# Optimization experiments

Hardware: AMD Instinct MI355X
Metric: run time of the kernel (lower is better)

## Reference

```python
import jax, jax.numpy as jnp
import numpy as np

B, D, C, T = 2, 1024, 256, 32
H = 8
F = C // H
E = 1024  # time_embed_dim
GROUPS = 32
SCALE = F ** -0.5


def group_norm(x, scale, bias):
    # x: [B, D, C, T]; GroupNorm(32, C) over (channels-in-group, T)
    b, d, c, t = x.shape
    xg = x.reshape(b, d, GROUPS, c // GROUPS, t)
    m = xg.mean(axis=(3, 4), keepdims=True)
    v = xg.var(axis=(3, 4), keepdims=True)
    xn = ((xg - m) * jax.lax.rsqrt(v + 1e-5)).reshape(b, d, c, t)
    return xn * scale[None, None, :, None] + bias[None, None, :, None]


def rpe_R(temb, pairwise, dw, db, tw, tb, ow, ob):
    # pairwise: [B, T, T] int -> R: [B, T, T, H, F]
    pd = pairwise.astype(jnp.float32)
    dist_embs = jnp.stack([
        jnp.log1p(jnp.maximum(pd, 0.0)),
        jnp.log1p(jnp.maximum(-pd, 0.0)),
        (pairwise == 0).astype(jnp.float32),
    ], axis=-1)  # [B, T, T, 3]
    emb = (temb @ tw.T + tb)[:, :, None, :] + (dist_embs @ dw.T + db)  # [B,T,T,C]
    r = jax.nn.silu(emb) @ ow.T + ob
    return r.reshape(r.shape[0], r.shape[1], r.shape[2], H, F)


def setup_inputs() -> dict:
    key = jax.random.key(0)
    ks = jax.random.split(key, 20)
    s = 0.02
    inp = {
        "x": jax.random.normal(ks[0], (B, D, C, T), jnp.float32),
        "temb": jax.random.normal(ks[1], (B, T, E), jnp.float32),
        "norm_scale": jnp.ones((C,), jnp.float32),
        "norm_bias": jnp.zeros((C,), jnp.float32),
        "qkv_w": jax.random.normal(ks[2], (3 * C, C), jnp.float32) * s,
        "qkv_b": jnp.zeros((3 * C,), jnp.float32),
        "proj_w": jax.random.normal(ks[3], (C, C), jnp.float32) * s,
        "proj_b": jnp.zeros((C,), jnp.float32),
        # stacked RPE params for (q, k, v) nets
        "rpe_dist_w": jax.random.normal(ks[4], (3, C, 3), jnp.float32) * s,
        "rpe_dist_b": jnp.zeros((3, C), jnp.float32),
        "rpe_time_w": jax.random.normal(ks[5], (3, C, E), jnp.float32) * s,
        "rpe_time_b": jnp.zeros((3, C), jnp.float32),
        "rpe_out_w": jax.random.normal(ks[6], (3, C, C), jnp.float32) * s,
        "rpe_out_b": jax.random.normal(ks[7], (3, C), jnp.float32) * s,
        "frame_indices": jnp.sort(jax.random.randint(ks[8], (B, T), 0, 100), axis=-1),
    }
    return inp


def reference(x, temb, norm_scale, norm_bias, qkv_w, qkv_b, proj_w, proj_b,
              rpe_dist_w, rpe_dist_b, rpe_time_w, rpe_time_b, rpe_out_w, rpe_out_b,
              frame_indices):
    xn = group_norm(x, norm_scale, norm_bias)          # [B,D,C,T]
    xt = jnp.einsum('BDCT->BDTC', xn)                  # [B,D,T,C]
    qkv = (xt @ qkv_w.T + qkv_b).reshape(B, D, T, 3, H, F)
    qkv = jnp.einsum('BDTtHF->tBDHTF', qkv)
    q, k, v = qkv[0] * SCALE, qkv[1], qkv[2]           # [B,D,H,T,F]

    attn = jnp.einsum('bdhtf,bdhsf->bdhts', q, k)

    pairwise = frame_indices[:, :, None] - frame_indices[:, None, :]  # [B,T,T]
    R_q = rpe_R(temb, pairwise, rpe_dist_w[0], rpe_dist_b[0], rpe_time_w[0], rpe_time_b[0], rpe_out_w[0], rpe_out_b[0])
    R_k = rpe_R(temb, pairwise, rpe_dist_w[1], rpe_dist_b[1], rpe_time_w[1], rpe_time_b[1], rpe_out_w[1], rpe_out_b[1])
    R_v = rpe_R(temb, pairwise, rpe_dist_w[2], rpe_dist_b[2], rpe_time_w[2], rpe_time_b[2], rpe_out_w[2], rpe_out_b[2])

    attn = attn + jnp.einsum('bdhtf,btshf->bdhts', q, R_k)
    # rpe_q: forward_qk on (k*scale) then transpose last two dims
    attn = attn + jnp.einsum('bdhtf,btshf->bdhts', k * SCALE, R_q).swapaxes(-1, -2)

    attn = jax.nn.softmax(attn.astype(jnp.float32), axis=-1).astype(attn.dtype)

    out = jnp.einsum('bdhts,bdhsf->bdhtf', attn, v)
    out = out + jnp.einsum('bdhts,btshf->bdhtf', attn, R_v)

    out = jnp.einsum('BDHTF->BDTHF', out).reshape(B, D, T, C)
    out = out @ proj_w.T + proj_b
    y = xt + out                                       # residual on post-norm x (as in source)
    return jnp.einsum('BDTC->BDCT', y)
```

## Files before the change

### kernel.cpp

```cpp
#include <hip/hip_runtime.h>

#define BB 2
#define DD 1024
#define CC 256
#define TT 32
#define HH 8
#define FF 32
#define EE 1024
#define SCALE 0.17677669529663687f

typedef unsigned short u16;
typedef unsigned int u32;
typedef __attribute__((ext_vector_type(8))) short s8v;
typedef __attribute__((ext_vector_type(4))) float f32x4;

static __device__ __forceinline__ float u2f(u16 u) {
  return __uint_as_float(((u32)u) << 16);
}
static __device__ __forceinline__ u16 f2u(float f) {
  u32 x = __float_as_uint(f);
  x += 0x7fffu + ((x >> 16) & 1u);
  return (u16)(x >> 16);
}
static __device__ __forceinline__ float dot2bf(u32 a, u32 b, float c) {
  float d;
  asm("v_dot2_f32_bf16 %0, %1, %2, %3" : "=v"(d) : "v"(a), "v"(b), "v"(c));
  return d;
}
#define D2(acc, a, b) acc = dot2bf(a, b, acc)

static __device__ __forceinline__ float logits_r(
    const u16* kr,
    uint4 r0, uint4 r1, uint4 r2, uint4 r3,
    uint4 r4, uint4 r5, uint4 r6, uint4 r7,
    uint4 q0, uint4 q1, uint4 q2, uint4 q3) {
  uint4 k0 = *(const uint4*)(kr + 0);
  uint4 k1 = *(const uint4*)(kr + 8);
  uint4 k2 = *(const uint4*)(kr + 16);
  uint4 k3 = *(const uint4*)(kr + 24);
  float xq = 0.f, xr = 0.f, xk = 0.f;
  D2(xq, q0.x, k0.x); D2(xq, q0.y, k0.y); D2(xq, q0.z, k0.z); D2(xq, q0.w, k0.w);
  D2(xq, q1.x, k1.x); D2(xq, q1.y, k1.y); D2(xq, q1.z, k1.z); D2(xq, q1.w, k1.w);
  D2(xq, q2.x, k2.x); D2(xq, q2.y, k2.y); D2(xq, q2.z, k2.z); D2(xq, q2.w, k2.w);
  D2(xq, q3.x, k3.x); D2(xq, q3.y, k3.y); D2(xq, q3.z, k3.z); D2(xq, q3.w, k3.w);
  D2(xr, q0.x, r0.x); D2(xr, q0.y, r0.y); D2(xr, q0.z, r0.z); D2(xr, q0.w, r0.w);
  D2(xr, q1.x, r1.x); D2(xr, q1.y, r1.y); D2(xr, q1.z, r1.z); D2(xr, q1.w, r1.w);
  D2(xr, q2.x, r2.x); D2(xr, q2.y, r2.y); D2(xr, q2.z, r2.z); D2(xr, q2.w, r2.w);
  D2(xr, q3.x, r3.x); D2(xr, q3.y, r3.y); D2(xr, q3.z, r3.z); D2(xr, q3.w, r3.w);
  D2(xk, k0.x, r4.x); D2(xk, k0.y, r4.y); D2(xk, k0.z, r4.z); D2(xk, k0.w, r4.w);
  D2(xk, k1.x, r5.x); D2(xk, k1.y, r5.y); D2(xk, k1.z, r5.z); D2(xk, k1.w, r5.w);
  D2(xk, k2.x, r6.x); D2(xk, k2.y, r6.y); D2(xk, k2.z, r6.z); D2(xk, k2.w, r6.w);
  D2(xk, k3.x, r7.x); D2(xk, k3.y, r7.y); D2(xk, k3.z, r7.z); D2(xk, k3.w, r7.w);
  return xq + xr + xk;
}

static __device__ __forceinline__ float pv_r(
    uint4 p0, uint4 p1, uint4 p2, uint4 p3,
    const u16* vr, uint4 r0, uint4 r1, uint4 r2, uint4 r3) {
  uint4 v0 = *(const uint4*)(vr + 0),  v1 = *(const uint4*)(vr + 8);
  uint4 v2 = *(const uint4*)(vr + 16), v3 = *(const uint4*)(vr + 24);
  float o = 0.f;
  D2(o, p0.x, v0.x); D2(o, p0.y, v0.y); D2(o, p0.z, v0.z); D2(o, p0.w, v0.w);
  D2(o, p1.x, v1.x); D2(o, p1.y, v1.y); D2(o, p1.z, v1.z); D2(o, p1.w, v1.w);
  D2(o, p2.x, v2.x); D2(o, p2.y, v2.y); D2(o, p2.z, v2.z); D2(o, p2.w, v2.w);
  D2(o, p3.x, v3.x); D2(o, p3.y, v3.y); D2(o, p3.z, v3.z); D2(o, p3.w, v3.w);
  D2(o, p0.x, r0.x); D2(o, p0.y, r0.y); D2(o, p0.z, r0.z); D2(o, p0.w, r0.w);
  D2(o, p1.x, r1.x); D2(o, p1.y, r1.y); D2(o, p1.z, r1.z); D2(o, p1.w, r1.w);
  D2(o, p2.x, r2.x); D2(o, p2.y, r2.y); D2(o, p2.z, r2.z); D2(o, p2.w, r2.w);
  D2(o, p3.x, r3.x); D2(o, p3.y, r3.y); D2(o, p3.z, r3.z); D2(o, p3.w, r3.w);
  return o;
}

#define LOADROW8(P, v0, v1, v2, v3, v4, v5, v6, v7)                      \
  v0 = *(const uint4*)((P) + 0);  v1 = *(const uint4*)((P) + 8);         \
  v2 = *(const uint4*)((P) + 16); v3 = *(const uint4*)((P) + 24);        \
  v4 = *(const uint4*)((P) + 32); v5 = *(const uint4*)((P) + 40);        \
  v6 = *(const uint4*)((P) + 48); v7 = *(const uint4*)((P) + 56);
#define LOADROW4(P, v0, v1, v2, v3)                                      \
  v0 = *(const uint4*)((P) + 0);  v1 = *(const uint4*)((P) + 8);         \
  v2 = *(const uint4*)((P) + 16); v3 = *(const uint4*)((P) + 24);

__global__ __launch_bounds__(256, 4) void k_f0(
    const float* __restrict__ x, const float* __restrict__ nsc,
    const float* __restrict__ nbi, u16* __restrict__ pun,
    const float* __restrict__ qw, const float* __restrict__ pw,
    const float* __restrict__ ow, const float* __restrict__ tw,
    const float* __restrict__ temb, const float* __restrict__ tb,
    const float* __restrict__ dw, const float* __restrict__ db,
    const int* __restrict__ fidx,
    u16* __restrict__ wpk2, u16* __restrict__ ppk, u16* __restrict__ opk,
    u16* __restrict__ E) {
  const int bid = blockIdx.x;
  const int tid = threadIdx.x;
  __shared__ u16 xt[TT][264];
  __shared__ float st[EE];
  __shared__ float base_s[CC];
  __shared__ int sfi[TT];

  if (bid < 2048) {
    int xcd = bid & 7, jj = bid >> 3;
    int b = xcd >> 2;
    int d = (xcd & 3) * 256 + jj;
    const size_t xbase = ((size_t)(b * DD + d)) * 8192;
    u16* xnp = pun + xbase * 2 + 8192;
    {
      const int c0 = tid >> 3, tq = tid & 7;
      for (int c = c0; c < CC; c += 32) {
        float4 v = *(const float4*)(x + xbase + (size_t)c * TT + tq * 4);
        xt[tq * 4 + 0][c] = f2u(v.x);
        xt[tq * 4 + 1][c] = f2u(v.y);
        xt[tq * 4 + 2][c] = f2u(v.z);
        xt[tq * 4 + 3][c] = f2u(v.w);
      }
    }
    __syncthreads();
    {
      const int c = tid;
      float s = 0.f, s2 = 0.f;
      for (int t = 0; t < TT; ++t) { float v = u2f(xt[t][c]); s += v; s2 += v * v; }
      s += __shfl_xor(s, 1); s2 += __shfl_xor(s2, 1);
      s += __shfl_xor(s, 2); s2 += __shfl_xor(s2, 2);
      s += __shfl_xor(s, 4); s2 += __shfl_xor(s2, 4);
      const float mean = s * (1.f / 256.f);
      const float var = s2 * (1.f / 256.f) - mean * mean;
      const float rs = rsqrtf(var + 1e-5f);
      const float scv = nsc[c] * rs;
      const float biv = nbi[c] - mean * scv;
      for (int t = 0; t < TT; ++t) xt[t][c] = f2u(u2f(xt[t][c]) * scv + biv);
    }
    __syncthreads();
#pragma unroll
    for (int it = 0; it < 4; ++it) {
      int u = it * 256 + tid;
      int t = u >> 5, c = (u & 31) * 8;
      *(uint4*)(xnp + (size_t)u * 8) = *(const uint4*)&xt[t][c];
    }
  } else if (bid < 2272) {
    int id = (bid - 2048) * 256 + tid;
    if (id < 24576) {
      int lane = id & 63, ks = (id >> 6) & 7, tile = id >> 9;
      int hh = tile / 6, r = tile % 6, sec = r >> 1, nt = r & 1;
      int nrow = sec * 256 + hh * 32 + nt * 16 + (lane & 15);
      int k = ks * 32 + (lane >> 4) * 8;
      const float* src = qw + (size_t)nrow * 256 + k;
      u16* dst = wpk2 + (size_t)id * 8;
#pragma unroll
      for (int e = 0; e < 8; ++e) dst[e] = f2u(src[e]);
    } else if (id < 32768) {
      int j = id - 24576;
      int lane = j & 63, ks = (j >> 6) & 7, nt = j >> 9;
      int row = nt * 16 + (lane & 15);
      int k = ks * 32 + (lane >> 4) * 8;
      const float* src = pw + (size_t)row * 256 + k;
      u16* dst = ppk + (size_t)j * 8;
#pragma unroll
      for (int e = 0; e < 8; ++e) dst[e] = f2u(src[e]);
    } else {
      int j = id - 32768;
      int lane = j & 63, ks = (j >> 6) & 7, g = j >> 9;
      int n = g >> 4, ntg = g & 15;
      int row = ntg * 16 + (lane & 15);
      int k = ks * 32 + (lane >> 4) * 8;
      const float* src = ow + ((size_t)n * 256 + row) * 256 + k;
      u16* dst = opk + (size_t)j * 8;
#pragma unroll
      for (int e = 0; e < 8; ++e) dst[e] = f2u(src[e]);
    }
  } else {
    int bid3 = bid - 2272;
    int t = bid3 & 31, b = (bid3 >> 5) & 1, n = bid3 >> 6;
    for (int e = tid; e < EE; e += 256)
      st[e] = temb[((size_t)b * TT + t) * EE + e];
    if (tid < TT) sfi[tid] = fidx[b * TT + tid];
    __syncthreads();
    const int g = tid & 7, cl = tid >> 3;
#pragma unroll
    for (int pass = 0; pass < 8; ++pass) {
      const int c = pass * 32 + cl;
      const float* wr = tw + ((size_t)n * 256 + c) * 1024 + g * 4;
      float acc = 0.f;
      for (int step = 0; step < 32; ++step) {
        float4 wv = *(const float4*)(wr + step * 32);
        float4 sv = *(const float4*)(st + g * 4 + step * 32);
        acc += sv.x * wv.x + sv.y * wv.y + sv.z * wv.z + sv.w * wv.w;
      }
      acc += __shfl_xor(acc, 1);
      acc += __shfl_xor(acc, 2);
      acc += __shfl_xor(acc, 4);
      if (g == 0) base_s[c] = acc;
    }
    __syncthreads();
    const int c = tid;
    float base = base_s[c] + tb[n * 256 + c] + db[n * 256 + c];
    float dw0 = dw[(n * 256 + c) * 3 + 0];
    float dw1 = dw[(n * 256 + c) * 3 + 1];
    float dw2 = dw[(n * 256 + c) * 3 + 2];
    int ft = sfi[t];
    u16* erow = E + ((size_t)n * 2048 + b * 1024 + t * 32) * 256 + c;
    for (int s = 0; s < TT; ++s) {
      int pd = ft - sfi[s];
      float d0 = log1pf((float)(pd > 0 ? pd : 0));
      float d1 = log1pf((float)(pd < 0 ? -pd : 0));
      float d2 = (pd == 0) ? 1.f : 0.f;
      float e = base + d0 * dw0 + d1 * dw1 + d2 * dw2;
      float se = e / (1.f + expf(-e));
      erow[(size_t)s * 256] = f2u(se);
    }
  }
}

__global__ __launch_bounds__(256) void k_rgemm(
    const u16* __restrict__ E, const u16* __restrict__ opk,
    const float* __restrict__ ob,
    u16* __restrict__ RKQ, u16* __restrict__ Rv) {
  int bid = blockIdx.x;
  int n = bid >> 6, rem = bid & 63;
  int mblk = rem >> 1, nblk = rem & 1;
  int tid = threadIdx.x;
  int w = tid >> 6, lane = tid & 63;
  int l15 = lane & 15, l4 = lane >> 4;
  size_t rowbase = (size_t)n * 2048 + mblk * 64;

  f32x4 acc[2][4];
#pragma unroll
  for (int i = 0; i < 2; ++i) {
    int ntg = nblk * 8 + w * 2 + i;
    float ov = ob[n * 256 + ntg * 16 + l15];
#pragma unroll
    for (int mt = 0; mt < 4; ++mt) acc[i][mt] = (f32x4){ov, ov, ov, ov};
  }
  for (int ks = 0; ks < 8; ++ks) {
    s8v a[4];
#pragma unroll
    for (int mt = 0; mt < 4; ++mt)
      a[mt] = *(const s8v*)(E + (rowbase + mt * 16 + l15) * 256 + ks * 32 + l4 * 8);
#pragma unroll
    for (int i = 0; i < 2; ++i) {
      int ntg = nblk * 8 + w * 2 + i;
      s8v bf = *(const s8v*)(opk + (((size_t)(n * 16 + ntg) * 8 + ks) * 64 + lane) * 8);
#pragma unroll
      for (int mt = 0; mt < 4; ++mt)
        acc[i][mt] = __builtin_amdgcn_mfma_f32_16x16x32_bf16(a[mt], bf, acc[i][mt], 0, 0, 0);
    }
  }
#pragma unroll
  for (int i = 0; i < 2; ++i) {
    int cc = (nblk * 8 + w * 2 + i) * 16 + l15;
    int hh = cc >> 5, f = cc & 31;
#pragma unroll
    for (int mt = 0; mt < 4; ++mt)
#pragma unroll
      for (int r = 0; r < 4; ++r) {
        int rloc = mblk * 64 + mt * 16 + l4 * 4 + r;
        int bb2 = rloc >> 10, tt = (rloc >> 5) & 31, ss = rloc & 31;
        size_t bh = (size_t)(bb2 * 8 + hh);
        float v = acc[i][mt][r];
        if (n == 0)      RKQ[(bh * 1024 + ss * 32 + tt) * 64 + 32 + f] = f2u(v * SCALE);
        else if (n == 1) RKQ[(bh * 1024 + tt * 32 + ss) * 64 + f] = f2u(v);
        else             Rv[((bh * 32 + tt) * 32 + f) * 32 + ss] = f2u(v);
      }
  }
}

__global__ __launch_bounds__(256, 3) void k_attn(
    u16* __restrict__ pun, const u16* __restrict__ wpk2,
    const float* __restrict__ qkb,
    const u16* __restrict__ RKQ, const u16* __restrict__ Rv) {
  int bid = blockIdx.x;
  int xcd = bid & 7, i5 = bid >> 3;
  int b = xcd >> 2;
  int h = i5 & 7;
  int dg = (xcd & 3) * 64 + (i5 >> 3);
  int d0 = dg * 4;
  const int tid = threadIdx.x;
  __shared__ u16 xsbuf[32 * 264];
  __shared__ u16 qs[4][32][40];
  __shared__ u16 ks_[4][32][40];
  __shared__ u16 vT[4][32][40];
#define XS_(r, c)   xsbuf[(r) * 264 + (c)]
#define ATSP(d, t)  (xsbuf + ((d) * 32 + (t)) * 40)

  const int w = tid >> 6, lane = tid & 63;
  const int l15 = lane & 15, l4 = lane >> 4;
  const int t = tid >> 3, j = tid & 7;
  const size_t bh = (size_t)(b * 8 + h);
  const u16* rp0 = RKQ + (bh * 1024 + (size_t)t * 32 + j) * 64;
  const u16* rv0 = Rv + ((bh * 32 + (size_t)t) * 32 + j) * 32;

  u16* slot0 = pun + ((size_t)(b * DD + d0)) * 16384;

  const u16* xp0 = slot0 + 8192;
  uint4 xr0 = *(const uint4*)(xp0 + (size_t)tid * 8);
  uint4 xr1 = *(const uint4*)(xp0 + (size_t)(256 + tid) * 8);
  uint4 xr2 = *(const uint4*)(xp0 + (size_t)(512 + tid) * 8);
  uint4 xr3 = *(const uint4*)(xp0 + (size_t)(768 + tid) * 8);

  s8v wf[3][8];
#pragma unroll
  for (int i = 0; i < 3; ++i) {
    const int u = w * 3 + i;
    const int sec = u >> 2, nt = (u >> 1) & 1;
    const u16* wb = wpk2 + ((size_t)((h * 6 + sec * 2 + nt) * 8) * 64 + lane) * 8;
#pragma unroll
    for (int ks = 0; ks < 8; ++ks)
      wf[i][ks] = *(const s8v*)(wb + (size_t)ks * 512);
  }

  for (int d = 0; d < 4; ++d) {
    *(uint4*)&XS_((tid >> 5), (tid & 31) * 8) = xr0;
    *(uint4*)&XS_(8 + (tid >> 5), (tid & 31) * 8) = xr1;
    *(uint4*)&XS_(16 + (tid >> 5), (tid & 31) * 8) = xr2;
    *(uint4*)&XS_(24 + (tid >> 5), (tid & 31) * 8) = xr3;
    __syncthreads();
    if (d < 3) {
      const u16* nx = slot0 + (size_t)(d + 1) * 16384 + 8192;
      xr0 = *(const uint4*)(nx + (size_t)tid * 8);
      xr1 = *(const uint4*)(nx + (size_t)(256 + tid) * 8);
      xr2 = *(const uint4*)(nx + (size_t)(512 + tid) * 8);
      xr3 = *(const uint4*)(nx + (size_t)(768 + tid) * 8);
    }
#pragma unroll
    for (int i = 0; i < 3; ++i) {
      const int u = w * 3 + i;
      const int sec = u >> 2;
      const int nt = (u >> 1) & 1;
      const int mh = u & 1;
      f32x4 acc = {0.f, 0.f, 0.f, 0.f};
#pragma unroll
      for (int ks = 0; ks < 8; ++ks) {
        s8v a = *(const s8v*)&XS_(mh * 16 + l15, ks * 32 + l4 * 8);
        acc = __builtin_amdgcn_mfma_f32_16x16x32_bf16(a, wf[i][ks], acc, 0, 0, 0);
      }
      const int f = nt * 16 + l15;
      const float bias = qkb[sec * 256 + h * 32 + f];
#pragma unroll
      for (int r = 0; r < 4; ++r) {
        const int tt = mh * 16 + l4 * 4 + r;
        const float val = acc[r] + bias;
        if (sec == 0)      qs[d][tt][f] = f2u(val * SCALE);
        else if (sec == 1) ks_[d][tt][f] = f2u(val);
        else               vT[d][f][tt] = f2u(val);
      }
    }
    __syncthreads();
  }

  uint4 q[4][4];
#pragma unroll
  for (int d = 0; d < 4; ++d) {
    q[d][0] = *(const uint4*)&qs[d][t][0];
    q[d][1] = *(const uint4*)&qs[d][t][8];
    q[d][2] = *(const uint4*)&qs[d][t][16];
    q[d][3] = *(const uint4*)&qs[d][t][24];
  }
  float a[4][4];
  uint4 A0, A1, A2, A3, A4, A5, A6, A7;
  uint4 B0, B1, B2, B3, B4, B5, B6, B7;
  LOADROW8(rp0,          A0, A1, A2, A3, A4, A5, A6, A7)
  LOADROW8(rp0 + 8 * 64, B0, B1, B2, B3, B4, B5, B6, B7)
#pragma unroll
  for (int d = 0; d < 4; ++d)
    a[d][0] = logits_r(&ks_[d][j][0], A0, A1, A2, A3, A4, A5, A6, A7,
                       q[d][0], q[d][1], q[d][2], q[d][3]);
  LOADROW8(rp0 + 16 * 64, A0, A1, A2, A3, A4, A5, A6, A7)
#pragma unroll
  for (int d = 0; d < 4; ++d)
    a[d][1] = logits_r(&ks_[d][j + 8][0], B0, B1, B2, B3, B4, B5, B6, B7,
                       q[d][0], q[d][1], q[d][2], q[d][3]);
  LOADROW8(rp0 + 24 * 64, B0, B1, B2, B3, B4, B5, B6, B7)
#pragma unroll
  for (int d = 0; d < 4; ++d)
    a[d][2] = logits_r(&ks_[d][j + 16][0], A0, A1, A2, A3, A4, A5, A6, A7,
                       q[d][0], q[d][1], q[d][2], q[d][3]);
#pragma unroll
  for (int d = 0; d < 4; ++d)
    a[d][3] = logits_r(&ks_[d][j + 24][0], B0, B1, B2, B3, B4, B5, B6, B7,
                       q[d][0], q[d][1], q[d][2], q[d][3]);

#pragma unroll
  for (int d = 0; d < 4; ++d) {
    float mx = fmaxf(fmaxf(a[d][0], a[d][1]), fmaxf(a[d][2], a[d][3]));
    mx = fmaxf(mx, __shfl_xor(mx, 1));
    mx = fmaxf(mx, __shfl_xor(mx, 2));
    mx = fmaxf(mx, __shfl_xor(mx, 4));
    float e0 = __expf(a[d][0] - mx), e1 = __expf(a[d][1] - mx);
    float e2 = __expf(a[d][2] - mx), e3 = __expf(a[d][3] - mx);
    float sum = e0 + e1 + e2 + e3;
    sum += __shfl_xor(sum, 1);
    sum += __shfl_xor(sum, 2);
    sum += __shfl_xor(sum, 4);
    const float inv = 1.f / sum;
    u16* ap = ATSP(d, t);
    ap[j]      = f2u(e0 * inv);
    ap[j + 8]  = f2u(e1 * inv);
    ap[j + 16] = f2u(e2 * inv);
    ap[j + 24] = f2u(e3 * inv);
  }

  uint4 p[4][4];
#pragma unroll
  for (int d = 0; d < 4; ++d) {
    const u16* ap = ATSP(d, t);
    p[d][0] = *(const uint4*)(ap + 0);
    p[d][1] = *(const uint4*)(ap + 8);
    p[d][2] = *(const uint4*)(ap + 16);
    p[d][3] = *(const uint4*)(ap + 24);
  }
  float o[4][4];
  uint4 VA0, VA1, VA2, VA3, VB0, VB1, VB2, VB3;
  LOADROW4(rv0,          VA0, VA1, VA2, VA3)
  LOADROW4(rv0 + 8 * 32, VB0, VB1, VB2, VB3)
#pragma unroll
  for (int d = 0; d < 4; ++d)
    o[d][0] = pv_r(p[d][0], p[d][1], p[d][2], p[d][3], &vT[d][j][0],
                   VA0, VA1, VA2, VA3);
  LOADROW4(rv0 + 16 * 32, VA0, VA1, VA2, VA3)
#pragma unroll
  for (int d = 0; d < 4; ++d)
    o[d][1] = pv_r(p[d][0], p[d][1], p[d][2], p[d][3], &vT[d][j + 8][0],
                   VB0, VB1, VB2, VB3);
  LOADROW4(rv0 + 24 * 32, VB0, VB1, VB2, VB3)
#pragma unroll
  for (int d = 0; d < 4; ++d)
    o[d][2] = pv_r(p[d][0], p[d][1], p[d][2], p[d][3], &vT[d][j + 16][0],
                   VA0, VA1, VA2, VA3);
#pragma unroll
  for (int d = 0; d < 4; ++d)
    o[d][3] = pv_r(p[d][0], p[d][1], p[d][2], p[d][3], &vT[d][j + 24][0],
                   VB0, VB1, VB2, VB3);

#pragma unroll
  for (int d = 0; d < 4; ++d) {
    u16* op = slot0 + (size_t)d * 16384 + (size_t)t * 256 + h * 32 + j;
    op[0]  = f2u(o[d][0]);
    op[8]  = f2u(o[d][1]);
    op[16] = f2u(o[d][2]);
    op[24] = f2u(o[d][3]);
  }
#undef XS_
#undef ATSP
}

__global__ __launch_bounds__(256, 4) void k_proj(
    u16* __restrict__ pun, const u16* __restrict__ ppk,
    const float* __restrict__ pb, float* __restrict__ out) {
  int bid = blockIdx.x;
  int xcd = bid & 7, jj = bid >> 3;
  int b = xcd >> 2;
  int d = (xcd & 3) * 256 + jj;
  const int tid = threadIdx.x;
  __shared__ u16 obuf[32][264];
  __shared__ u16 xs[32][264];
  const size_t nbase = ((size_t)(b * DD + d)) * 8192;
  u16* slot = pun + nbase * 2;
#pragma unroll
  for (int it = 0; it < 4; ++it) {
    int u = it * 256 + tid;
    int t = u >> 5, c = (u & 31) * 8;
    *(uint4*)&obuf[t][c] = *(const uint4*)(slot + (size_t)u * 8);
    *(uint4*)&xs[t][c]   = *(const uint4*)(slot + 8192 + (size_t)u * 8);
  }
  __syncthreads();

  const int w = tid >> 6, lane = tid & 63;
  const int l15 = lane & 15, l4 = lane >> 4;
  f32x4 pacc[4][2];
#pragma unroll
  for (int i = 0; i < 4; ++i) {
    pacc[i][0] = (f32x4){0.f, 0.f, 0.f, 0.f};
    pacc[i][1] = (f32x4){0.f, 0.f, 0.f, 0.f};
  }
  for (int ks = 0; ks < 8; ++ks) {
    s8v a0 = *(const s8v*)&obuf[l15][ks * 32 + l4 * 8];
    s8v a1 = *(const s8v*)&obuf[16 + l15][ks * 32 + l4 * 8];
#pragma unroll
    for (int i = 0; i < 4; ++i) {
      s8v bf = *(const s8v*)(ppk + ((size_t)((w * 4 + i) * 8 + ks) * 64 + lane) * 8);
      pacc[i][0] = __builtin_amdgcn_mfma_f32_16x16x32_bf16(a0, bf, pacc[i][0], 0, 0, 0);
      pacc[i][1] = __builtin_amdgcn_mfma_f32_16x16x32_bf16(a1, bf, pacc[i][1], 0, 0, 0);
    }
  }
#pragma unroll
  for (int i = 0; i < 4; ++i) {
    const int co = (w * 4 + i) * 16 + l15;
    const float pbv = pb[co];
#pragma unroll
    for (int mt = 0; mt < 2; ++mt) {
      const int t0 = mt * 16 + l4 * 4;
      float4 sv;
      sv.x = pacc[i][mt][0] + u2f(xs[t0 + 0][co]) + pbv;
      sv.y = pacc[i][mt][1] + u2f(xs[t0 + 1][co]) + pbv;
      sv.z = pacc[i][mt][2] + u2f(xs[t0 + 2][co]) + pbv;
      sv.w = pacc[i][mt][3] + u2f(xs[t0 + 3][co]) + pbv;
      *(float4*)(out + nbase + (size_t)co * TT + t0) = sv;
    }
  }
}

extern "C" void kernel_launch(void* const* d_in, const int* in_sizes, int n_in,
                              void* d_out, int out_size, void* d_ws, size_t ws_size,
                              hipStream_t stream) {
  const float* x      = (const float*)d_in[0];
  const float* temb   = (const float*)d_in[1];
  const float* nsc    = (const float*)d_in[2];
  const float* nbi    = (const float*)d_in[3];
  const float* qkv_w  = (const float*)d_in[4];
  const float* qkv_b  = (const float*)d_in[5];
  const float* proj_w = (const float*)d_in[6];
  const float* proj_b = (const float*)d_in[7];
  const float* dw     = (const float*)d_in[8];
  const float* db     = (const float*)d_in[9];
  const float* tw     = (const float*)d_in[10];
  const float* tb     = (const float*)d_in[11];
  const float* ow     = (const float*)d_in[12];
  const float* ob     = (const float*)d_in[13];
  const int*   fidx   = (const int*)d_in[14];
  float* out = (float*)d_out;
  u16* pun = (u16*)d_out;

  u16* wpk2 = (u16*)d_ws;
  u16* ppk  = wpk2 + 196608;
  u16* opk  = ppk + 65536;
  u16* E    = opk + 196608;
  u16* RKQ  = E + 1572864;
  u16* Rv   = RKQ + 1048576;

  k_f0<<<2464, 256, 0, stream>>>(x, nsc, nbi, pun, qkv_w, proj_w, ow, tw,
                                 temb, tb, dw, db, fidx, wpk2, ppk, opk, E);
  k_rgemm<<<192, 256, 0, stream>>>(E, opk, ob, RKQ, Rv);
  k_attn<<<4096, 256, 0, stream>>>(pun, wpk2, qkv_b, RKQ, Rv);
  k_proj<<<2048, 256, 0, stream>>>(pun, ppk, proj_b, out);
}
```

Before: 236.4 us.

## Drop LDS staging of x in attention QKV stage and raise occupancy

The QKV projection inside k_attn now reads its MFMA A operands straight from global memory and reloads the weight fragments per tile, instead of staging x through a shared-memory buffer and holding weights in registers. The x staging buffer is removed, and the probability scratch (ATSP) now aliases the qs array. The per-iteration barriers collapse into a single barrier after the loop, and launch bounds rise from 3 to 5 blocks per CU. The aim is to cut LDS use, register pressure and synchronization so more waves can hide latency. In exchange, each block makes more global/L2 traffic, including redundant weight loads. Loads also go directly from global to MFMA with no prefetch pipelining.

Measured after the change: 531.9 us. 125% more time.

```diff
diff --git a/kernel.cpp b/kernel.cpp
--- a/kernel.cpp
+++ b/kernel.cpp
@@ -262,7 +262,7 @@
   }
 }
 
-__global__ __launch_bounds__(256, 3) void k_attn(
+__global__ __launch_bounds__(256, 5) void k_attn(
     u16* __restrict__ pun, const u16* __restrict__ wpk2,
     const float* __restrict__ qkb,
     const u16* __restrict__ RKQ, const u16* __restrict__ Rv) {
@@ -273,12 +273,10 @@
   int dg = (xcd & 3) * 64 + (i5 >> 3);
   int d0 = dg * 4;
   const int tid = threadIdx.x;
-  __shared__ u16 xsbuf[32 * 264];
   __shared__ u16 qs[4][32][40];
   __shared__ u16 ks_[4][32][40];
   __shared__ u16 vT[4][32][40];
-#define XS_(r, c)   xsbuf[(r) * 264 + (c)]
-#define ATSP(d, t)  (xsbuf + ((d) * 32 + (t)) * 40)
+#define ATSP(d, t)  (&qs[d][t][0])
 
   const int w = tid >> 6, lane = tid & 63;
   const int l15 = lane & 15, l4 = lane >> 4;
@@ -289,36 +287,8 @@
 
   u16* slot0 = pun + ((size_t)(b * DD + d0)) * 16384;
 
-  const u16* xp0 = slot0 + 8192;
-  uint4 xr0 = *(const uint4*)(xp0 + (size_t)tid * 8);
-  uint4 xr1 = *(const uint4*)(xp0 + (size_t)(256 + tid) * 8);
-  uint4 xr2 = *(const uint4*)(xp0 + (size_t)(512 + tid) * 8);
-  uint4 xr3 = *(const uint4*)(xp0 + (size_t)(768 + tid) * 8);
-
-  s8v wf[3][8];
-#pragma unroll
-  for (int i = 0; i < 3; ++i) {
-    const int u = w * 3 + i;
-    const int sec = u >> 2, nt = (u >> 1) & 1;
-    const u16* wb = wpk2 + ((size_t)((h * 6 + sec * 2 + nt) * 8) * 64 + lane) * 8;
-#pragma unroll
-    for (int ks = 0; ks < 8; ++ks)
-      wf[i][ks] = *(const s8v*)(wb + (size_t)ks * 512);
-  }
-
   for (int d = 0; d < 4; ++d) {
-    *(uint4*)&XS_((tid >> 5), (tid & 31) * 8) = xr0;
-    *(uint4*)&XS_(8 + (tid >> 5), (tid & 31) * 8) = xr1;
-    *(uint4*)&XS_(16 + (tid >> 5), (tid & 31) * 8) = xr2;
-    *(uint4*)&XS_(24 + (tid >> 5), (tid & 31) * 8) = xr3;
-    __syncthreads();
-    if (d < 3) {
-      const u16* nx = slot0 + (size_t)(d + 1) * 16384 + 8192;
-      xr0 = *(const uint4*)(nx + (size_t)tid * 8);
-      xr1 = *(const uint4*)(nx + (size_t)(256 + tid) * 8);
-      xr2 = *(const uint4*)(nx + (size_t)(512 + tid) * 8);
-      xr3 = *(const uint4*)(nx + (size_t)(768 + tid) * 8);
-    }
+    const u16* xg = slot0 + (size_t)d * 16384 + 8192;
 #pragma unroll
     for (int i = 0; i < 3; ++i) {
       const int u = w * 3 + i;
@@ -326,10 +296,13 @@
       const int nt = (u >> 1) & 1;
       const int mh = u & 1;
       f32x4 acc = {0.f, 0.f, 0.f, 0.f};
+      const u16* wb = wpk2 + ((size_t)((h * 6 + sec * 2 + nt) * 8) * 64 + lane) * 8;
+      const u16* ag = xg + (size_t)(mh * 16 + l15) * 256 + l4 * 8;
 #pragma unroll
       for (int ks = 0; ks < 8; ++ks) {
-        s8v a = *(const s8v*)&XS_(mh * 16 + l15, ks * 32 + l4 * 8);
-        acc = __builtin_amdgcn_mfma_f32_16x16x32_bf16(a, wf[i][ks], acc, 0, 0, 0);
+        s8v a = *(const s8v*)(ag + ks * 32);
+        s8v bf = *(const s8v*)(wb + (size_t)ks * 512);
+        acc = __builtin_amdgcn_mfma_f32_16x16x32_bf16(a, bf, acc, 0, 0, 0);
       }
       const int f = nt * 16 + l15;
       const float bias = qkb[sec * 256 + h * 32 + f];
@@ -342,8 +315,8 @@
         else               vT[d][f][tt] = f2u(val);
       }
     }
-    __syncthreads();
-  }
+  }
+  __syncthreads();
 
   uint4 q[4][4];
 #pragma unroll
@@ -437,7 +410,6 @@
     op[16] = f2u(o[d][2]);
     op[24] = f2u(o[d][3]);
   }
-#undef XS_
 #undef ATSP
 }
 
```
